# Kernel tuning notes

Hardware: AMD Instinct MI355X
Metric: run time of the kernel (lower is better)

Reference implementation:

```python
import jax, jax.numpy as jnp
import numpy as np

B = 65536
H = 128          # hidden_size
IN_BOT = 128     # input_bottom_size
IN_TOP = 128     # input_top_size
GATE_W = 4 * H + 1  # 513: 4 gate chunks + 1 boundary logit
HARD_A = 1.0
ROUND_TH = 0.5


def setup_inputs() -> dict:
    key = jax.random.key(0)
    ks = jax.random.split(key, 10)
    sd = 1.0 / np.sqrt(H)
    return {
        "h_bottom": jax.random.normal(ks[0], (B, IN_BOT), jnp.float32),
        "h":        jax.random.normal(ks[1], (B, H), jnp.float32),
        "h_top":    jax.random.normal(ks[2], (B, IN_TOP), jnp.float32),
        "c":        jax.random.normal(ks[3], (B, H), jnp.float32),
        "z":        jax.random.randint(ks[4], (B, 1), 0, 2).astype(jnp.float32),
        "z_bottom": jax.random.randint(ks[5], (B, 1), 0, 2).astype(jnp.float32),
        "W": jax.random.uniform(ks[6], (IN_BOT, GATE_W), jnp.float32, -sd, sd),
        "R": jax.random.uniform(ks[7], (H, GATE_W), jnp.float32, -sd, sd),
        "U": jax.random.uniform(ks[8], (IN_TOP, GATE_W), jnp.float32, -sd, sd),
        "b": jax.random.uniform(ks[9], (GATE_W,), jnp.float32, -sd, sd),
    }


def _hard_sigm(x, a=HARD_A):
    # HardSigm: clip((a*x + 1)/2, 0, 1)
    return jnp.clip((a * x + 1.0) * 0.5, 0.0, 1.0)


def _round_st(z_tilde, th=ROUND_TH):
    # threshold rounding with straight-through gradient (identity backward)
    hard = (z_tilde > th).astype(z_tilde.dtype)
    return z_tilde + jax.lax.stop_gradient(hard - z_tilde)


def reference(h_bottom, h, h_top, c, z, z_bottom, W, R, U, b):
    # fused gate pre-activations: [B, 4H+1]
    s = (h_bottom * z_bottom) @ W + h @ R + (h_top * z) @ U + b
    si = s[:, 0 * H:1 * H]
    sg = s[:, 1 * H:2 * H]
    so = s[:, 2 * H:3 * H]
    sf = s[:, 3 * H:4 * H]
    sz = s[:, 4 * H:4 * H + 1]
    i = jax.nn.sigmoid(si)
    g = jnp.tanh(sg)
    o = jax.nn.sigmoid(so)
    f = jax.nn.sigmoid(sf)
    ig = i * g
    # FLUSH if z==1; COPY if z==0 & z_bottom==0; UPDATE otherwise
    c_new = jnp.where(z == 1.0, ig, jnp.where(z_bottom == 0.0, c, c * f + ig))
    h_new = jnp.where((z == 0.0) & (z_bottom == 0.0), h, jnp.tanh(c_new) * o)
    z_new = _round_st(_hard_sigm(sz))
    return (h_new, c_new, z_new)
```

## Files before the change

kernel.cpp:

```cpp
#include <hip/hip_runtime.h>
#include <hip/hip_bf16.h>


#define MT   64
#define BK   32
#define NKC  12
#define NT   512
#define COFF 8388608
#define ZOFF 16777216

using short8 = __attribute__((ext_vector_type(8))) short;
using f32x4  = __attribute__((ext_vector_type(4))) float;

__device__ __forceinline__ unsigned short f2bf(float f) {
  union { float f; unsigned u; } v; v.f = f;
  unsigned r = (v.u + 0x7FFFu + ((v.u >> 16) & 1u)) >> 16;
  return (unsigned short)r;
}

__device__ __forceinline__ void async_copy16(const void* g, void* l) {
  __builtin_amdgcn_global_load_lds(
      (const __attribute__((address_space(1))) unsigned int*)g,
      (__attribute__((address_space(3))) unsigned int*)l, 16, 0, 0);
}

__device__ __forceinline__ float sigm(float x)     { return 1.f / (1.f + __expf(-x)); }
__device__ __forceinline__ float tanh_fast(float x){ return 1.f - 2.f / (1.f + __expf(2.f * x)); }

__global__ void prep_weights(const float* __restrict__ W, const float* __restrict__ R,
                             const float* __restrict__ U, unsigned short* __restrict__ Wt) {
  int idx = blockIdx.x * blockDim.x + threadIdx.x;
  if (idx >= NKC * 512 * 4) return;
  int up = idx & 3;
  int n  = (idx >> 2) & 511;
  int c  = idx >> 11;
  int ul = up ^ ((n >> 1) & 3);
  int k0 = c * 32 + ul * 8;
  const float* src; int kb;
  if (k0 < 128)      { src = W; kb = 0;   }
  else if (k0 < 256) { src = R; kb = 128; }
  else               { src = U; kb = 256; }
  const float* colp = src + (size_t)(k0 - kb) * 513 + n;
  unsigned short vs[8];
  #pragma unroll
  for (int j = 0; j < 8; ++j) vs[j] = f2bf(colp[j * 513]);
  uint4 o;
  o.x = (unsigned)vs[0] | ((unsigned)vs[1] << 16);
  o.y = (unsigned)vs[2] | ((unsigned)vs[3] << 16);
  o.z = (unsigned)vs[4] | ((unsigned)vs[5] << 16);
  o.w = (unsigned)vs[6] | ((unsigned)vs[7] << 16);
  reinterpret_cast<uint4*>(Wt)[idx] = o;
}

__global__ __launch_bounds__(NT, 4)
void hmlstm_main(const float* __restrict__ hb, const float* __restrict__ hs,
                 const float* __restrict__ ht, const float* __restrict__ cs,
                 const float* __restrict__ zp, const float* __restrict__ zbp,
                 const float* __restrict__ W,  const float* __restrict__ R,
                 const float* __restrict__ U,  const float* __restrict__ b,
                 const unsigned short* __restrict__ Wt, float* __restrict__ out)
{
  __shared__ unsigned short ldsW[2][512 * BK];
  __shared__ unsigned short ldsA[2][MT * BK];
  __shared__ float  ldsWL[384];
  __shared__ double ldsSZ[NT];

  const int tid  = threadIdx.x;
  const int l    = tid & 63;
  const int wv   = tid >> 6;
  const int ws   = wv & 3;
  const int wr   = wv >> 2;
  const int q    = l >> 4;
  const int lr   = l & 15;
  const int row0 = blockIdx.x * MT;

  for (int k = tid; k < 384; k += NT) {
    ldsWL[k] = (k < 128) ? W[k * 513 + 512]
             : (k < 256) ? R[(k - 128) * 513 + 512]
                         : U[(k - 256) * 513 + 512];
  }

  const int m    = tid >> 3;
  const int p    = tid & 7;
  const int arow = row0 + m;
  const float zbv = zbp[arow];
  const float zv  = zp[arow];
  double szacc = 0.0;

  f32x4 acc[2][8];
  {
    f32x4 zf = {0.f, 0.f, 0.f, 0.f};
    #pragma unroll
    for (int i = 0; i < 2; ++i)
      #pragma unroll
      for (int j = 0; j < 8; ++j) acc[i][j] = zf;
  }

  const int aW = m * BK + (((p >> 1) ^ ((m >> 1) & 3)) * 8) + (p & 1) * 4;
  const size_t rowb = (size_t)arow * 128 + p * 4;

  auto loadA = [&](int c) -> f32x4 {
    const float* src = (c < 4) ? hb : (c < 8) ? hs : ht;
    return *(const f32x4*)(src + rowb + (c & 3) * 32);
  };
  auto consumeA = [&](int c, f32x4 v, int buf) {
    const float scale = (c < 4) ? zbv : (c < 8) ? 1.f : zv;
    v *= scale;
    const float* wl = ldsWL + c * 32 + p * 4;
    szacc += (double)v.x * wl[0] + (double)v.y * wl[1]
           + (double)v.z * wl[2] + (double)v.w * wl[3];
    uint2 pk;
    pk.x = (unsigned)f2bf(v.x) | ((unsigned)f2bf(v.y) << 16);
    pk.y = (unsigned)f2bf(v.z) | ((unsigned)f2bf(v.w) << 16);
    *(uint2*)&ldsA[buf][aW] = pk;
  };
  auto stageW = [&](int c, int buf) {
    const unsigned short* gW = Wt + c * (512 * BK);
    #pragma unroll
    for (int r = 0; r < 4; ++r) {
      int eo = (wv * 4 + r) * 512;
      async_copy16(gW + eo + l * 8, &ldsW[buf][eo]);
    }
  };

  f32x4 a0 = loadA(0);
  asm volatile("s_waitcnt lgkmcnt(0)" ::: "memory");
  __builtin_amdgcn_s_barrier();
  consumeA(0, a0, 0);
  stageW(0, 0);
  f32x4 ain = loadA(1);
  stageW(1, 1);
  asm volatile("s_waitcnt vmcnt(5)" ::: "memory");
  asm volatile("s_waitcnt lgkmcnt(0)" ::: "memory");
  __builtin_amdgcn_s_barrier();

  #pragma unroll 1
  for (int kc = 0; kc < NKC; ++kc) {
    const int cur = kc & 1;
    short8 af[2];
    #pragma unroll
    for (int s = 0; s < 2; ++s) {
      int mr = wr * 32 + s * 16 + lr;
      af[s] = *(const short8*)&ldsA[cur][mr * BK + ((q ^ ((mr >> 1) & 3)) * 8)];
    }
    #pragma unroll
    for (int tn = 0; tn < 8; ++tn) {
      int nc = (tn >> 1) * 128 + ws * 32 + (tn & 1) * 16 + lr;
      short8 bf = *(const short8*)&ldsW[cur][nc * BK + ((q ^ ((nc >> 1) & 3)) * 8)];
      acc[0][tn] = __builtin_amdgcn_mfma_f32_16x16x32_bf16(af[0], bf, acc[0][tn], 0, 0, 0);
      acc[1][tn] = __builtin_amdgcn_mfma_f32_16x16x32_bf16(af[1], bf, acc[1][tn], 0, 0, 0);
    }
    if (kc < NKC - 1) {
      consumeA(kc + 1, ain, cur ^ 1);
      if (kc < NKC - 2) {
        ain = loadA(kc + 2);
        asm volatile("s_waitcnt vmcnt(1)" ::: "memory");
      } else {
        asm volatile("s_waitcnt vmcnt(0)" ::: "memory");
      }
      asm volatile("s_waitcnt lgkmcnt(0)" ::: "memory");
      __builtin_amdgcn_s_barrier();
      if (kc < NKC - 2) stageW(kc + 2, cur);
    }
  }

  ldsSZ[tid] = szacc;
  __syncthreads();
  if (tid < MT) {
    const double* pz = &ldsSZ[tid * 8];
    double ss = ((pz[0] + pz[1]) + (pz[2] + pz[3])) + ((pz[4] + pz[5]) + (pz[6] + pz[7]));
    float s = (float)ss + b[512];
    out[ZOFF + row0 + tid] = (s > 0.f) ? 1.f : 0.f;
  }

  float bias[2][4];
  #pragma unroll
  for (int th = 0; th < 2; ++th) {
    const int col = ws * 32 + th * 16 + lr;
    bias[th][0] = b[col];       bias[th][1] = b[128 + col];
    bias[th][2] = b[256 + col]; bias[th][3] = b[384 + col];
  }
  #pragma unroll
  for (int s = 0; s < 2; ++s) {
    #pragma unroll
    for (int r = 0; r < 4; ++r) {
      const int row = row0 + wr * 32 + s * 16 + q * 4 + r;
      const float zr  = zp[row];
      const float zbr = zbp[row];
      const size_t rowoff = (size_t)row * 128;
      #pragma unroll
      for (int th = 0; th < 2; ++th) {
        const int col = ws * 32 + th * 16 + lr;
        const size_t off = rowoff + col;
        float si = acc[s][0 + th][r] + bias[th][0];
        float sg = acc[s][2 + th][r] + bias[th][1];
        float so = acc[s][4 + th][r] + bias[th][2];
        float sf = acc[s][6 + th][r] + bias[th][3];
        float iv = sigm(si);
        float gv = tanh_fast(sg);
        float ov = sigm(so);
        float fv = sigm(sf);
        float ig = iv * gv;
        float cv = cs[off];
        float hv = hs[off];
        float cn = (zr == 1.f) ? ig : ((zbr == 0.f) ? cv : cv * fv + ig);
        float hn = (zr == 0.f && zbr == 0.f) ? hv : tanh_fast(cn) * ov;
        out[off]        = hn;
        out[COFF + off] = cn;
      }
    }
  }
}

extern "C" void kernel_launch(void* const* d_in, const int* in_sizes, int n_in,
                              void* d_out, int out_size, void* d_ws, size_t ws_size,
                              hipStream_t stream) {
  const float* hb  = (const float*)d_in[0];
  const float* hs  = (const float*)d_in[1];
  const float* ht  = (const float*)d_in[2];
  const float* cs  = (const float*)d_in[3];
  const float* zp  = (const float*)d_in[4];
  const float* zbp = (const float*)d_in[5];
  const float* W   = (const float*)d_in[6];
  const float* R   = (const float*)d_in[7];
  const float* U   = (const float*)d_in[8];
  const float* b   = (const float*)d_in[9];
  unsigned short* Wt = (unsigned short*)d_ws;
  float* out = (float*)d_out;

  prep_weights<<<dim3(96), dim3(256), 0, stream>>>(W, R, U, Wt);
  hmlstm_main<<<dim3(65536 / MT), dim3(NT), 0, stream>>>(
      hb, hs, ht, cs, zp, zbp, W, R, U, b, Wt, out);
}
```

Baseline: 226.1 us.

## Load weight fragments directly into registers instead of staging through LDS

Removes the LDS double-buffered weight staging and has each wave read its bf16 weight fragments straight from global memory into registers, prefetching the next K-chunk. The wave tiling changes so each wave covers all 64 rows and 16 columns of each gate, and the prep kernel's swizzle is dropped to match. The epilogue also skips loading c and h when the flags make them unused. This cuts LDS traffic and LDS footprint at the cost of more global and L2 weight reads per wave, plus a fully unrolled K loop that raises register pressure.

```diff
diff --git a/kernel.cpp b/kernel.cpp
--- a/kernel.cpp
+++ b/kernel.cpp
@@ -18,12 +18,6 @@
   return (unsigned short)r;
 }
 
-__device__ __forceinline__ void async_copy16(const void* g, void* l) {
-  __builtin_amdgcn_global_load_lds(
-      (const __attribute__((address_space(1))) unsigned int*)g,
-      (__attribute__((address_space(3))) unsigned int*)l, 16, 0, 0);
-}
-
 __device__ __forceinline__ float sigm(float x)     { return 1.f / (1.f + __expf(-x)); }
 __device__ __forceinline__ float tanh_fast(float x){ return 1.f - 2.f / (1.f + __expf(2.f * x)); }
 
@@ -31,11 +25,10 @@
                              const float* __restrict__ U, unsigned short* __restrict__ Wt) {
   int idx = blockIdx.x * blockDim.x + threadIdx.x;
   if (idx >= NKC * 512 * 4) return;
-  int up = idx & 3;
+  int u  = idx & 3;
   int n  = (idx >> 2) & 511;
   int c  = idx >> 11;
-  int ul = up ^ ((n >> 1) & 3);
-  int k0 = c * 32 + ul * 8;
+  int k0 = c * 32 + u * 8;
   const float* src; int kb;
   if (k0 < 128)      { src = W; kb = 0;   }
   else if (k0 < 256) { src = R; kb = 128; }
@@ -60,7 +53,6 @@
                  const float* __restrict__ U,  const float* __restrict__ b,
                  const unsigned short* __restrict__ Wt, float* __restrict__ out)
 {
-  __shared__ unsigned short ldsW[2][512 * BK];
   __shared__ unsigned short ldsA[2][MT * BK];
   __shared__ float  ldsWL[384];
   __shared__ double ldsSZ[NT];
@@ -68,8 +60,6 @@
   const int tid  = threadIdx.x;
   const int l    = tid & 63;
   const int wv   = tid >> 6;
-  const int ws   = wv & 3;
-  const int wr   = wv >> 2;
   const int q    = l >> 4;
   const int lr   = l & 15;
   const int row0 = blockIdx.x * MT;
@@ -87,13 +77,13 @@
   const float zv  = zp[arow];
   double szacc = 0.0;
 
-  f32x4 acc[2][8];
+  f32x4 acc[4][4];
   {
     f32x4 zf = {0.f, 0.f, 0.f, 0.f};
     #pragma unroll
-    for (int i = 0; i < 2; ++i)
-      #pragma unroll
-      for (int j = 0; j < 8; ++j) acc[i][j] = zf;
+    for (int i = 0; i < 4; ++i)
+      #pragma unroll
+      for (int j = 0; j < 4; ++j) acc[i][j] = zf;
   }
 
   const int aW = m * BK + (((p >> 1) ^ ((m >> 1) & 3)) * 8) + (p & 1) * 4;
@@ -114,53 +104,48 @@
     pk.y = (unsigned)f2bf(v.z) | ((unsigned)f2bf(v.w) << 16);
     *(uint2*)&ldsA[buf][aW] = pk;
   };
-  auto stageW = [&](int c, int buf) {
-    const unsigned short* gW = Wt + c * (512 * BK);
-    #pragma unroll
-    for (int r = 0; r < 4; ++r) {
-      int eo = (wv * 4 + r) * 512;
-      async_copy16(gW + eo + l * 8, &ldsW[buf][eo]);
-    }
-  };
+
+  const unsigned short* wp = Wt + (wv * 16 + lr) * 32 + q * 8;
 
   f32x4 a0 = loadA(0);
   asm volatile("s_waitcnt lgkmcnt(0)" ::: "memory");
   __builtin_amdgcn_s_barrier();
   consumeA(0, a0, 0);
-  stageW(0, 0);
   f32x4 ain = loadA(1);
-  stageW(1, 1);
-  asm volatile("s_waitcnt vmcnt(5)" ::: "memory");
+  short8 wf[4];
+  #pragma unroll
+  for (int g = 0; g < 4; ++g)
+    wf[g] = *(const short8*)(wp + g * 4096);
   asm volatile("s_waitcnt lgkmcnt(0)" ::: "memory");
   __builtin_amdgcn_s_barrier();
 
-  #pragma unroll 1
+  #pragma unroll
   for (int kc = 0; kc < NKC; ++kc) {
     const int cur = kc & 1;
-    short8 af[2];
-    #pragma unroll
-    for (int s = 0; s < 2; ++s) {
-      int mr = wr * 32 + s * 16 + lr;
+    short8 af[4];
+    #pragma unroll
+    for (int s = 0; s < 4; ++s) {
+      int mr = s * 16 + lr;
       af[s] = *(const short8*)&ldsA[cur][mr * BK + ((q ^ ((mr >> 1) & 3)) * 8)];
     }
-    #pragma unroll
-    for (int tn = 0; tn < 8; ++tn) {
-      int nc = (tn >> 1) * 128 + ws * 32 + (tn & 1) * 16 + lr;
-      short8 bf = *(const short8*)&ldsW[cur][nc * BK + ((q ^ ((nc >> 1) & 3)) * 8)];
-      acc[0][tn] = __builtin_amdgcn_mfma_f32_16x16x32_bf16(af[0], bf, acc[0][tn], 0, 0, 0);
-      acc[1][tn] = __builtin_amdgcn_mfma_f32_16x16x32_bf16(af[1], bf, acc[1][tn], 0, 0, 0);
-    }
+    short8 wn[4];
     if (kc < NKC - 1) {
+      #pragma unroll
+      for (int g = 0; g < 4; ++g)
+        wn[g] = *(const short8*)(wp + (kc + 1) * 16384 + g * 4096);
       consumeA(kc + 1, ain, cur ^ 1);
-      if (kc < NKC - 2) {
-        ain = loadA(kc + 2);
-        asm volatile("s_waitcnt vmcnt(1)" ::: "memory");
-      } else {
-        asm volatile("s_waitcnt vmcnt(0)" ::: "memory");
-      }
+      if (kc < NKC - 2) ain = loadA(kc + 2);
+    }
+    #pragma unroll
+    for (int s = 0; s < 4; ++s)
+      #pragma unroll
+      for (int g = 0; g < 4; ++g)
+        acc[s][g] = __builtin_amdgcn_mfma_f32_16x16x32_bf16(af[s], wf[g], acc[s][g], 0, 0, 0);
+    if (kc < NKC - 1) {
+      #pragma unroll
+      for (int g = 0; g < 4; ++g) wf[g] = wn[g];
       asm volatile("s_waitcnt lgkmcnt(0)" ::: "memory");
       __builtin_amdgcn_s_barrier();
-      if (kc < NKC - 2) stageW(kc + 2, cur);
     }
   }
 
@@ -173,41 +158,33 @@
     out[ZOFF + row0 + tid] = (s > 0.f) ? 1.f : 0.f;
   }
 
-  float bias[2][4];
-  #pragma unroll
-  for (int th = 0; th < 2; ++th) {
-    const int col = ws * 32 + th * 16 + lr;
-    bias[th][0] = b[col];       bias[th][1] = b[128 + col];
-    bias[th][2] = b[256 + col]; bias[th][3] = b[384 + col];
-  }
-  #pragma unroll
-  for (int s = 0; s < 2; ++s) {
+  const int col = wv * 16 + lr;
+  const float b0 = b[col], b1 = b[128 + col], b2 = b[256 + col], b3 = b[384 + col];
+  #pragma unroll
+  for (int s = 0; s < 4; ++s) {
     #pragma unroll
     for (int r = 0; r < 4; ++r) {
-      const int row = row0 + wr * 32 + s * 16 + q * 4 + r;
+      const int row = row0 + s * 16 + q * 4 + r;
       const float zr  = zp[row];
       const float zbr = zbp[row];
-      const size_t rowoff = (size_t)row * 128;
-      #pragma unroll
-      for (int th = 0; th < 2; ++th) {
-        const int col = ws * 32 + th * 16 + lr;
-        const size_t off = rowoff + col;
-        float si = acc[s][0 + th][r] + bias[th][0];
-        float sg = acc[s][2 + th][r] + bias[th][1];
-        float so = acc[s][4 + th][r] + bias[th][2];
-        float sf = acc[s][6 + th][r] + bias[th][3];
-        float iv = sigm(si);
-        float gv = tanh_fast(sg);
-        float ov = sigm(so);
-        float fv = sigm(sf);
-        float ig = iv * gv;
-        float cv = cs[off];
-        float hv = hs[off];
-        float cn = (zr == 1.f) ? ig : ((zbr == 0.f) ? cv : cv * fv + ig);
-        float hn = (zr == 0.f && zbr == 0.f) ? hv : tanh_fast(cn) * ov;
-        out[off]        = hn;
-        out[COFF + off] = cn;
-      }
+      const size_t off = (size_t)row * 128 + col;
+      float si = acc[s][0][r] + b0;
+      float sg = acc[s][1][r] + b1;
+      float so = acc[s][2][r] + b2;
+      float sf = acc[s][3][r] + b3;
+      float iv = sigm(si);
+      float gv = tanh_fast(sg);
+      float ov = sigm(so);
+      float fv = sigm(sf);
+      float ig = iv * gv;
+      float cv = 0.f, hv = 0.f;
+      if (zr != 1.f) cv = cs[off];
+      const bool keep = (zr == 0.f) && (zbr == 0.f);
+      if (keep) hv = hs[off];
+      float cn = (zr == 1.f) ? ig : ((zbr == 0.f) ? cv : cv * fv + ig);
+      float hn = keep ? hv : tanh_fast(cn) * ov;
+      out[off]        = hn;
+      out[COFF + off] = cn;
     }
   }
 }
```

New measurement: 323.8 us. 43.2% more time.

## Load weight fragments directly into registers instead of staging through LDS

Applied to the files above, without the earlier changes.

Reorders the pre-packed bf16 weight layout so each lane can load its MFMA B-fragments straight from global memory into registers. This removes the double-buffered LDS weight tiles and the async global-to-LDS copies, which cuts LDS use and should allow more resident blocks per CU. Each wave now re-reads weights from global/L2 every k-chunk, with less explicit latency hiding since the vmcnt waits are gone. The epilogue also skips loading c when z==1 and skips loading h unless it is the copy case, saving memory reads.

```diff
diff --git a/kernel.cpp b/kernel.cpp
--- a/kernel.cpp
+++ b/kernel.cpp
@@ -18,12 +18,6 @@
   return (unsigned short)r;
 }
 
-__device__ __forceinline__ void async_copy16(const void* g, void* l) {
-  __builtin_amdgcn_global_load_lds(
-      (const __attribute__((address_space(1))) unsigned int*)g,
-      (__attribute__((address_space(3))) unsigned int*)l, 16, 0, 0);
-}
-
 __device__ __forceinline__ float sigm(float x)     { return 1.f / (1.f + __expf(-x)); }
 __device__ __forceinline__ float tanh_fast(float x){ return 1.f - 2.f / (1.f + __expf(2.f * x)); }
 
@@ -31,11 +25,13 @@
                              const float* __restrict__ U, unsigned short* __restrict__ Wt) {
   int idx = blockIdx.x * blockDim.x + threadIdx.x;
   if (idx >= NKC * 512 * 4) return;
-  int up = idx & 3;
-  int n  = (idx >> 2) & 511;
+  int u  = idx & 3;
+  int x  = (idx >> 2) & 15;
+  int tn = (idx >> 6) & 7;
+  int s  = (idx >> 9) & 3;
   int c  = idx >> 11;
-  int ul = up ^ ((n >> 1) & 3);
-  int k0 = c * 32 + ul * 8;
+  int n  = (tn >> 1) * 128 + s * 32 + (tn & 1) * 16 + x;
+  int k0 = c * 32 + u * 8;
   const float* src; int kb;
   if (k0 < 128)      { src = W; kb = 0;   }
   else if (k0 < 256) { src = R; kb = 128; }
@@ -60,7 +56,6 @@
                  const float* __restrict__ U,  const float* __restrict__ b,
                  const unsigned short* __restrict__ Wt, float* __restrict__ out)
 {
-  __shared__ unsigned short ldsW[2][512 * BK];
   __shared__ unsigned short ldsA[2][MT * BK];
   __shared__ float  ldsWL[384];
   __shared__ double ldsSZ[NT];
@@ -114,23 +109,18 @@
     pk.y = (unsigned)f2bf(v.z) | ((unsigned)f2bf(v.w) << 16);
     *(uint2*)&ldsA[buf][aW] = pk;
   };
-  auto stageW = [&](int c, int buf) {
-    const unsigned short* gW = Wt + c * (512 * BK);
-    #pragma unroll
-    for (int r = 0; r < 4; ++r) {
-      int eo = (wv * 4 + r) * 512;
-      async_copy16(gW + eo + l * 8, &ldsW[buf][eo]);
-    }
-  };
+
+  const unsigned short* wkc = Wt + (size_t)ws * 4096 + lr * 32 + q * 8;
 
   f32x4 a0 = loadA(0);
+  short8 wf[8];
+  #pragma unroll
+  for (int tn = 0; tn < 8; ++tn)
+    wf[tn] = *(const short8*)(wkc + tn * 512);
   asm volatile("s_waitcnt lgkmcnt(0)" ::: "memory");
   __builtin_amdgcn_s_barrier();
   consumeA(0, a0, 0);
-  stageW(0, 0);
   f32x4 ain = loadA(1);
-  stageW(1, 1);
-  asm volatile("s_waitcnt vmcnt(5)" ::: "memory");
   asm volatile("s_waitcnt lgkmcnt(0)" ::: "memory");
   __builtin_amdgcn_s_barrier();
 
@@ -145,22 +135,18 @@
     }
     #pragma unroll
     for (int tn = 0; tn < 8; ++tn) {
-      int nc = (tn >> 1) * 128 + ws * 32 + (tn & 1) * 16 + lr;
-      short8 bf = *(const short8*)&ldsW[cur][nc * BK + ((q ^ ((nc >> 1) & 3)) * 8)];
-      acc[0][tn] = __builtin_amdgcn_mfma_f32_16x16x32_bf16(af[0], bf, acc[0][tn], 0, 0, 0);
-      acc[1][tn] = __builtin_amdgcn_mfma_f32_16x16x32_bf16(af[1], bf, acc[1][tn], 0, 0, 0);
+      acc[0][tn] = __builtin_amdgcn_mfma_f32_16x16x32_bf16(af[0], wf[tn], acc[0][tn], 0, 0, 0);
+      acc[1][tn] = __builtin_amdgcn_mfma_f32_16x16x32_bf16(af[1], wf[tn], acc[1][tn], 0, 0, 0);
     }
     if (kc < NKC - 1) {
+      #pragma unroll
+      for (int tn = 0; tn < 8; ++tn)
+        wf[tn] = *(const short8*)(wkc + 16384 + tn * 512);
       consumeA(kc + 1, ain, cur ^ 1);
-      if (kc < NKC - 2) {
-        ain = loadA(kc + 2);
-        asm volatile("s_waitcnt vmcnt(1)" ::: "memory");
-      } else {
-        asm volatile("s_waitcnt vmcnt(0)" ::: "memory");
-      }
+      if (kc < NKC - 2) ain = loadA(kc + 2);
+      wkc += 16384;
       asm volatile("s_waitcnt lgkmcnt(0)" ::: "memory");
       __builtin_amdgcn_s_barrier();
-      if (kc < NKC - 2) stageW(kc + 2, cur);
     }
   }
 
@@ -201,10 +187,12 @@
         float ov = sigm(so);
         float fv = sigm(sf);
         float ig = iv * gv;
-        float cv = cs[off];
-        float hv = hs[off];
+        float cv = 0.f, hv = 0.f;
+        if (zr != 1.f) cv = cs[off];
+        const bool keep = (zr == 0.f) && (zbr == 0.f);
+        if (keep) hv = hs[off];
         float cn = (zr == 1.f) ? ig : ((zbr == 0.f) ? cv : cv * fv + ig);
-        float hn = (zr == 0.f && zbr == 0.f) ? hv : tanh_fast(cn) * ov;
+        float hn = keep ? hv : tanh_fast(cn) * ov;
         out[off]        = hn;
         out[COFF + off] = cn;
       }
```

Measured after the change: 249.9 us. 1.11x slower.
